# Performance work log

Measured on AMD Instinct MI355X. Metric: run time of the kernel, lower is better.

## Reference

```python
import jax, jax.numpy as jnp
import numpy as np
import math

NUM_HEADS = 16

def _skew(QEr):
    # QEr: [B, H, S, S] -> pad 1 on left of last dim, reshape, drop first row
    B, H, S, _ = QEr.shape
    padded = jnp.pad(QEr, ((0, 0), (0, 0), (0, 0), (1, 0)))  # [B,H,S,S+1]
    reshaped = padded.reshape(B, H, S + 1, S)
    return reshaped[:, :, 1:, :]  # [B,H,S,S]

def setup_inputs() -> dict:
    key = jax.random.key(0)
    ks = jax.random.split(key, 8)
    B, S, D, dh = 4, 1024, 1024, 64
    x = jax.random.normal(ks[0], (B, S, D), dtype=jnp.float32)
    scale = 1.0 / math.sqrt(D)
    Wq = jax.random.normal(ks[1], (D, D), dtype=jnp.float32) * scale
    Wk = jax.random.normal(ks[2], (D, D), dtype=jnp.float32) * scale
    Wv = jax.random.normal(ks[3], (D, D), dtype=jnp.float32) * scale
    bq = jnp.zeros((D,), dtype=jnp.float32)
    bk = jnp.zeros((D,), dtype=jnp.float32)
    bv = jnp.zeros((D,), dtype=jnp.float32)
    Er = jax.random.normal(ks[4], (S, dh), dtype=jnp.float32)
    return {"x": x, "Wq": Wq, "bq": bq, "Wk": Wk, "bk": bk, "Wv": Wv, "bv": bv, "Er": Er}

def reference(x, Wq, bq, Wk, bk, Wv, bv, Er):
    B, S, D = x.shape
    H = NUM_HEADS
    dh = D // H
    # Linear projections (torch Linear: x @ W.T + b)
    q = (x @ Wq.T + bq).reshape(B, S, H, dh).transpose(0, 2, 1, 3)  # [B,H,S,dh]
    k = (x @ Wk.T + bk).reshape(B, S, H, dh).transpose(0, 2, 1, 3)
    v = (x @ Wv.T + bv).reshape(B, S, H, dh).transpose(0, 2, 1, 3)
    # Relative position term: q @ Er^T then skew (start = max_len - S = 0)
    QEr = jnp.einsum('bhsd,td->bhst', q, Er)  # [B,H,S,S]
    Srel = _skew(QEr)
    QKt = jnp.einsum('bhsd,bhtd->bhst', q, k)  # [B,H,S,S]
    attn = (QKt + Srel) / math.sqrt(dh)
    causal = jnp.tril(jnp.ones((S, S), dtype=bool))
    attn = jnp.where(causal[None, None], attn, jnp.float32(-1e6))
    attn = jax.nn.softmax(attn, axis=-1)
    out = jnp.einsum('bhst,bhtd->bhsd', attn, v)  # [B,H,S,dh]
    out = out.transpose(0, 2, 1, 3).reshape(B, S, D)
    return out  # dropout is identity in eval / p=0
```

## Files before the change

### kernel.cpp

```cpp
#include <hip/hip_runtime.h>
#include <stdint.h>

#define S_LEN 1024
#define DM 1024
#define NH 16
#define DH 64
#define NB 4

typedef unsigned short u16;
typedef __attribute__((ext_vector_type(8))) short short8;
typedef __attribute__((ext_vector_type(4))) float f32x4;
typedef __attribute__((ext_vector_type(4))) unsigned int u32x4;

__device__ __forceinline__ u16 f2bf(float f) {
  union { float f; unsigned int u; } c;
  c.f = f;
  unsigned int u = c.u;
  return (u16)((u + 0x7fffu + ((u >> 16) & 1u)) >> 16);
}

__device__ __forceinline__ void g2l16(const void* g, void* l) {
  __builtin_amdgcn_global_load_lds(
      (const __attribute__((address_space(1))) unsigned int*)(uintptr_t)g,
      (__attribute__((address_space(3))) unsigned int*)(uint32_t)(uintptr_t)l,
      16, 0, 0);
}

__global__ __launch_bounds__(256) void cvt_f32_bf16(
    const float* __restrict__ x, const float* __restrict__ Wq,
    const float* __restrict__ Wk, const float* __restrict__ Wv,
    const float* __restrict__ Er, u16* __restrict__ xb,
    u16* __restrict__ Wqb, u16* __restrict__ Wkb, u16* __restrict__ Wvb,
    u16* __restrict__ Erb) {
  const size_t f = ((size_t)blockIdx.x * 256 + threadIdx.x) * 8;
  const float* src;
  u16* dst;
  size_t off;
  if (f < 4194304) { src = x; dst = xb; off = f; }
  else if (f < 5242880) { src = Wq; dst = Wqb; off = f - 4194304; }
  else if (f < 6291456) { src = Wk; dst = Wkb; off = f - 5242880; }
  else if (f < 7340032) { src = Wv; dst = Wvb; off = f - 6291456; }
  else { src = Er; dst = Erb; off = f - 7340032; }
  const float4 a = *(const float4*)(src + off);
  const float4 b = *(const float4*)(src + off + 4);
  u16 o[8] = {f2bf(a.x), f2bf(a.y), f2bf(a.z), f2bf(a.w),
              f2bf(b.x), f2bf(b.y), f2bf(b.z), f2bf(b.w)};
  *(u32x4*)(dst + off) = *(const u32x4*)o;
}

__global__ __launch_bounds__(256) void qkv_gemm(
    const u16* __restrict__ x,
    const u16* __restrict__ Wq, const float* __restrict__ bq,
    const u16* __restrict__ Wk, const float* __restrict__ bk,
    const u16* __restrict__ Wv, const float* __restrict__ bv,
    u16* __restrict__ Qo, u16* __restrict__ Ko, u16* __restrict__ Vo) {
  __shared__ __attribute__((aligned(16))) u16 Al[128 * 32];
  __shared__ __attribute__((aligned(16))) u16 Bl[128 * 32];

  const int tid = threadIdx.x;
  const int lane = tid & 63;
  const int wave = tid >> 6;
  const int z = blockIdx.z;
  const u16* W = (z == 0) ? Wq : (z == 1) ? Wk : Wv;
  const float* bias = (z == 0) ? bq : (z == 1) ? bk : bv;

  const int m0 = blockIdx.y * 128;
  const int n0 = blockIdx.x * 128;

  f32x4 acc[4][4];
  const f32x4 fzero = {0.f, 0.f, 0.f, 0.f};
#pragma unroll
  for (int i = 0; i < 4; i++)
#pragma unroll
    for (int j = 0; j < 4; j++) acc[i][j] = fzero;

  const int srow = tid >> 2;
  const int schunk = tid & 3;
  const u16* gA = x + (size_t)(m0 + srow) * DM + schunk * 8;
  const u16* gB = W + (size_t)(n0 + srow) * DM + schunk * 8;

  const int fr = lane & 15;
  const int fq = lane >> 4;
  const int wr = (wave >> 1) * 64;
  const int wc = (wave & 1) * 64;

  for (int k = 0; k < DM; k += 32) {
    g2l16(gA + k, &Al[tid * 8]);
    g2l16(gA + (size_t)64 * DM + k, &Al[2048 + tid * 8]);
    g2l16(gB + k, &Bl[tid * 8]);
    g2l16(gB + (size_t)64 * DM + k, &Bl[2048 + tid * 8]);
    __syncthreads();
    short8 a[4], b[4];
#pragma unroll
    for (int i = 0; i < 4; i++)
      a[i] = *(const short8*)&Al[(wr + i * 16 + fr) * 32 + fq * 8];
#pragma unroll
    for (int j = 0; j < 4; j++)
      b[j] = *(const short8*)&Bl[(wc + j * 16 + fr) * 32 + fq * 8];
#pragma unroll
    for (int i = 0; i < 4; i++)
#pragma unroll
      for (int j = 0; j < 4; j++)
        acc[i][j] =
            __builtin_amdgcn_mfma_f32_16x16x32_bf16(a[i], b[j], acc[i][j], 0, 0, 0);
    __syncthreads();
  }

#pragma unroll
  for (int j = 0; j < 4; j++) {
    const int n = n0 + wc + j * 16 + fr;
    const float bsv = bias[n];
    const int h = n >> 6, d = n & (DH - 1);
#pragma unroll
    for (int i = 0; i < 4; i++) {
#pragma unroll
      for (int r = 0; r < 4; r++) {
        const int m = m0 + wr + i * 16 + fq * 4 + r;
        const int bb = m >> 10, s = m & (S_LEN - 1);
        const u16 o = f2bf(acc[i][j][r] + bsv);
        if (z == 2)
          Vo[((size_t)(bb * NH + h) * DH + d) * S_LEN + s] = o;
        else if (z == 1)
          Ko[((size_t)(bb * NH + h) * S_LEN + s) * DH + d] = o;
        else
          Qo[((size_t)(bb * NH + h) * S_LEN + s) * DH + d] = o;
      }
    }
  }
}

__global__ __launch_bounds__(512, 4) void attn(
    const u16* __restrict__ Q, const u16* __restrict__ K,
    const u16* __restrict__ Vt, const u16* __restrict__ Er,
    float* __restrict__ out) {
  __shared__ __attribute__((aligned(16))) u16 El[192 * 72];
  __shared__ __attribute__((aligned(16))) u16 Kl[64 * 72];
  __shared__ __attribute__((aligned(16))) u16 Vl[64 * 72];
  __shared__ __attribute__((aligned(16))) u16 Pl[8 * 16 * 72];

  const int tid = threadIdx.x;
  const int lane = tid & 63;
  const int w = tid >> 6;
  const int bh = blockIdx.y;
  const int b = bh >> 4, h = bh & (NH - 1);
  const int it = (blockIdx.y < 32) ? (int)blockIdx.x : 7 - (int)blockIdx.x;
  const int i0 = it * 128;

  const u16* Qb = Q + (size_t)bh * S_LEN * DH;
  const u16* Kb = K + (size_t)bh * S_LEN * DH;
  const u16* Vb = Vt + (size_t)bh * DH * S_LEN;
  u16* Pw = Pl + w * 16 * 72;

  const int sr = tid >> 3;
  const int sc = (tid & 7) * 8;

  *(u32x4*)&El[sr * 72 + sc] = *(const u32x4*)&Qb[(i0 + sr) * DH + sc];
  *(u32x4*)&El[(sr + 64) * 72 + sc] =
      *(const u32x4*)&Qb[(i0 + sr + 64) * DH + sc];
  __syncthreads();

  const int fr = lane & 15;
  const int fq = lane >> 4;
  short8 aq0 = *(const short8*)&El[(w * 16 + fr) * 72 + fq * 8];
  short8 aq1 = *(const short8*)&El[(w * 16 + fr) * 72 + 32 + fq * 8];
  __syncthreads();

  float mrow[4], lrow[4];
  f32x4 accO[4];
  const f32x4 fzero = {0.f, 0.f, 0.f, 0.f};
#pragma unroll
  for (int r = 0; r < 4; r++) { mrow[r] = -3.0e38f; lrow[r] = 0.f; }
#pragma unroll
  for (int t = 0; t < 4; t++) accO[t] = fzero;

  for (int j0 = 0; j0 <= i0 + 64; j0 += 64) {
    *(u32x4*)&Kl[sr * 72 + sc] = *(const u32x4*)&Kb[(j0 + sr) * DH + sc];
    *(u32x4*)&Vl[sr * 72 + sc] = *(const u32x4*)&Vb[sr * S_LEN + j0 + sc];
    const int E0 = S_LEN - 128 - i0 + j0;
#pragma unroll
    for (int qq = 0; qq < 3; qq++) {
      const int g = sr + 64 * qq;
      int e = E0 + g;
      e = (e > S_LEN - 1) ? (S_LEN - 1) : e;
      *(u32x4*)&El[g * 72 + sc] = *(const u32x4*)&Er[e * DH + sc];
    }
    __syncthreads();

    if (j0 <= i0 + w * 16 + 15) {
      f32x4 sfr[4];
#pragma unroll
      for (int t = 0; t < 4; t++) {
        short8 b0 = *(const short8*)&Kl[(t * 16 + fr) * 72 + fq * 8];
        short8 b1 = *(const short8*)&Kl[(t * 16 + fr) * 72 + 32 + fq * 8];
        f32x4 zz = fzero;
        zz = __builtin_amdgcn_mfma_f32_16x16x32_bf16(aq0, b0, zz, 0, 0, 0);
        zz = __builtin_amdgcn_mfma_f32_16x16x32_bf16(aq1, b1, zz, 0, 0, 0);
        sfr[t] = zz;
      }

      f32x4 zz[5];
#pragma unroll
      for (int f = 0; f < 5; f++) {
        const int er = 112 - w * 16 + f * 16 + fr;
        short8 b0 = *(const short8*)&El[er * 72 + fq * 8];
        short8 b1 = *(const short8*)&El[er * 72 + 32 + fq * 8];
        f32x4 t0 = fzero;
        t0 = __builtin_amdgcn_mfma_f32_16x16x32_bf16(aq0, b0, t0, 0, 0, 0);
        t0 = __builtin_amdgcn_mfma_f32_16x16x32_bf16(aq1, b1, t0, 0, 0, 0);
        zz[f] = t0;
      }

      float p[4][4];
#pragma unroll
      for (int r = 0; r < 4; r++) {
        const int row = fq * 4 + r;
        const int c = 15 - row + fr;
        const int src = (fq << 4) | (c & 15);
        float sh[5];
#pragma unroll
        for (int f = 0; f < 5; f++) sh[f] = __shfl(zz[f][r], src);
#pragma unroll
        for (int t = 0; t < 4; t++) {
          const float rel = (c < 16) ? sh[t] : sh[t + 1];
          float sv = (sfr[t][r] + rel) * 0.125f;
          const int jj = j0 + t * 16 + fr;
          const int ii = i0 + w * 16 + row;
          if (jj > ii) sv = -3.0e38f;
          p[t][r] = sv;
        }
      }

#pragma unroll
      for (int r = 0; r < 4; r++) {
        float rm = fmaxf(fmaxf(p[0][r], p[1][r]), fmaxf(p[2][r], p[3][r]));
#pragma unroll
        for (int off = 1; off < 16; off <<= 1)
          rm = fmaxf(rm, __shfl_xor(rm, off));
        const float mnew = fmaxf(mrow[r], rm);
        const float alpha = __expf(mrow[r] - mnew);
        mrow[r] = mnew;
        float rs = 0.f;
#pragma unroll
        for (int t = 0; t < 4; t++) {
          const float e = __expf(p[t][r] - mnew);
          p[t][r] = e;
          rs += e;
        }
#pragma unroll
        for (int off = 1; off < 16; off <<= 1) rs += __shfl_xor(rs, off);
        lrow[r] = lrow[r] * alpha + rs;
#pragma unroll
        for (int t = 0; t < 4; t++) accO[t][r] *= alpha;
      }

#pragma unroll
      for (int t = 0; t < 4; t++)
#pragma unroll
        for (int r = 0; r < 4; r++)
          Pw[(fq * 4 + r) * 72 + t * 16 + fr] = f2bf(p[t][r]);
      __builtin_amdgcn_s_waitcnt(0xC07F);

      short8 ap0 = *(const short8*)&Pw[fr * 72 + fq * 8];
      short8 ap1 = *(const short8*)&Pw[fr * 72 + 32 + fq * 8];
#pragma unroll
      for (int t = 0; t < 4; t++) {
        short8 b0 = *(const short8*)&Vl[(t * 16 + fr) * 72 + fq * 8];
        short8 b1 = *(const short8*)&Vl[(t * 16 + fr) * 72 + 32 + fq * 8];
        accO[t] =
            __builtin_amdgcn_mfma_f32_16x16x32_bf16(ap0, b0, accO[t], 0, 0, 0);
        accO[t] =
            __builtin_amdgcn_mfma_f32_16x16x32_bf16(ap1, b1, accO[t], 0, 0, 0);
      }
    }
    __syncthreads();
  }

#pragma unroll
  for (int r = 0; r < 4; r++) {
    const float inv = 1.f / lrow[r];
    const int s = i0 + w * 16 + fq * 4 + r;
#pragma unroll
    for (int t = 0; t < 4; t++) {
      const int d = t * 16 + fr;
      out[((size_t)b * S_LEN + s) * DM + h * DH + d] = accO[t][r] * inv;
    }
  }
}

extern "C" void kernel_launch(void* const* d_in, const int* in_sizes, int n_in,
                              void* d_out, int out_size, void* d_ws, size_t ws_size,
                              hipStream_t stream) {
  const float* x = (const float*)d_in[0];
  const float* Wq = (const float*)d_in[1];
  const float* bq = (const float*)d_in[2];
  const float* Wk = (const float*)d_in[3];
  const float* bk = (const float*)d_in[4];
  const float* Wv = (const float*)d_in[5];
  const float* bv = (const float*)d_in[6];
  const float* Er = (const float*)d_in[7];
  float* out = (float*)d_out;

  const size_t per = (size_t)NB * NH * S_LEN * DH;
  u16* Qw = (u16*)d_ws;
  u16* Kw = Qw + per;
  u16* Vw = Kw + per;
  u16* xb = Vw + per;
  u16* Wqb = xb + per;
  u16* Wkb = Wqb + (size_t)DM * DM;
  u16* Wvb = Wkb + (size_t)DM * DM;
  u16* Erb = Wvb + (size_t)DM * DM;

  cvt_f32_bf16<<<3616, 256, 0, stream>>>(x, Wq, Wk, Wv, Er, xb, Wqb, Wkb, Wvb,
                                         Erb);
  dim3 g1(DM / 128, (NB * S_LEN) / 128, 3);
  qkv_gemm<<<g1, dim3(256), 0, stream>>>(xb, Wqb, bq, Wkb, bk, Wvb, bv, Qw, Kw,
                                         Vw);
  dim3 g2(8, NB * NH);
  attn<<<g2, dim3(512), 0, stream>>>(Qw, Kw, Vw, Erb, out);
}
```

Baseline: 179.5 us.

## Load attention K/V/Er fragments directly from global memory, dropping LDS staging

The attention kernel no longer stages Q, K, V and Er tiles in shared memory with block-wide barriers. Each wave loads its MFMA operand fragments straight from global memory, relying on L1/L2 caching, and loops only up to its own causal limit. This removes the __syncthreads and LDS traffic and lets waves progress independently. The cost is that every wave re-fetches K/V/Er fragments from global memory, which adds cache traffic and latency that is no longer amortized across the 8 waves of a block. The tile order for reversing the row-block sweep now alternates by head parity instead of by the batch half.

Result: slower. 300.6 us (+67.5%).

```diff
diff --git a/kernel.cpp b/kernel.cpp
--- a/kernel.cpp
+++ b/kernel.cpp
@@ -133,17 +133,15 @@
     const u16* __restrict__ Q, const u16* __restrict__ K,
     const u16* __restrict__ Vt, const u16* __restrict__ Er,
     float* __restrict__ out) {
-  __shared__ __attribute__((aligned(16))) u16 El[192 * 72];
-  __shared__ __attribute__((aligned(16))) u16 Kl[64 * 72];
-  __shared__ __attribute__((aligned(16))) u16 Vl[64 * 72];
   __shared__ __attribute__((aligned(16))) u16 Pl[8 * 16 * 72];
 
   const int tid = threadIdx.x;
   const int lane = tid & 63;
   const int w = tid >> 6;
+  const int bx = blockIdx.x;
   const int bh = blockIdx.y;
   const int b = bh >> 4, h = bh & (NH - 1);
-  const int it = (blockIdx.y < 32) ? (int)blockIdx.x : 7 - (int)blockIdx.x;
+  const int it = (bh & 1) ? 7 - bx : bx;
   const int i0 = it * 128;
 
   const u16* Qb = Q + (size_t)bh * S_LEN * DH;
@@ -151,19 +149,12 @@
   const u16* Vb = Vt + (size_t)bh * DH * S_LEN;
   u16* Pw = Pl + w * 16 * 72;
 
-  const int sr = tid >> 3;
-  const int sc = (tid & 7) * 8;
-
-  *(u32x4*)&El[sr * 72 + sc] = *(const u32x4*)&Qb[(i0 + sr) * DH + sc];
-  *(u32x4*)&El[(sr + 64) * 72 + sc] =
-      *(const u32x4*)&Qb[(i0 + sr + 64) * DH + sc];
-  __syncthreads();
-
   const int fr = lane & 15;
   const int fq = lane >> 4;
-  short8 aq0 = *(const short8*)&El[(w * 16 + fr) * 72 + fq * 8];
-  short8 aq1 = *(const short8*)&El[(w * 16 + fr) * 72 + 32 + fq * 8];
-  __syncthreads();
+
+  const u16* qrow = Qb + (size_t)(i0 + w * 16 + fr) * DH;
+  short8 aq0 = *(const short8*)&qrow[fq * 8];
+  short8 aq1 = *(const short8*)&qrow[32 + fq * 8];
 
   float mrow[4], lrow[4];
   f32x4 accO[4];
@@ -173,106 +164,98 @@
 #pragma unroll
   for (int t = 0; t < 4; t++) accO[t] = fzero;
 
-  for (int j0 = 0; j0 <= i0 + 64; j0 += 64) {
-    *(u32x4*)&Kl[sr * 72 + sc] = *(const u32x4*)&Kb[(j0 + sr) * DH + sc];
-    *(u32x4*)&Vl[sr * 72 + sc] = *(const u32x4*)&Vb[sr * S_LEN + j0 + sc];
-    const int E0 = S_LEN - 128 - i0 + j0;
-#pragma unroll
-    for (int qq = 0; qq < 3; qq++) {
-      const int g = sr + 64 * qq;
-      int e = E0 + g;
+  const int jmax = i0 + w * 16 + 15;
+  for (int j0 = 0; j0 <= jmax; j0 += 64) {
+    f32x4 sfr[4];
+#pragma unroll
+    for (int t = 0; t < 4; t++) {
+      const u16* kp = Kb + (size_t)(j0 + t * 16 + fr) * DH;
+      short8 b0 = *(const short8*)&kp[fq * 8];
+      short8 b1 = *(const short8*)&kp[32 + fq * 8];
+      f32x4 zt = fzero;
+      zt = __builtin_amdgcn_mfma_f32_16x16x32_bf16(aq0, b0, zt, 0, 0, 0);
+      zt = __builtin_amdgcn_mfma_f32_16x16x32_bf16(aq1, b1, zt, 0, 0, 0);
+      sfr[t] = zt;
+    }
+
+    const int E0 = 896 - i0 + j0;
+    f32x4 zz[5];
+#pragma unroll
+    for (int f = 0; f < 5; f++) {
+      int e = E0 + 112 - w * 16 + f * 16 + fr;
       e = (e > S_LEN - 1) ? (S_LEN - 1) : e;
-      *(u32x4*)&El[g * 72 + sc] = *(const u32x4*)&Er[e * DH + sc];
-    }
-    __syncthreads();
-
-    if (j0 <= i0 + w * 16 + 15) {
-      f32x4 sfr[4];
+      const u16* ep = Er + (size_t)e * DH;
+      short8 b0 = *(const short8*)&ep[fq * 8];
+      short8 b1 = *(const short8*)&ep[32 + fq * 8];
+      f32x4 t0 = fzero;
+      t0 = __builtin_amdgcn_mfma_f32_16x16x32_bf16(aq0, b0, t0, 0, 0, 0);
+      t0 = __builtin_amdgcn_mfma_f32_16x16x32_bf16(aq1, b1, t0, 0, 0, 0);
+      zz[f] = t0;
+    }
+
+    float p[4][4];
+#pragma unroll
+    for (int r = 0; r < 4; r++) {
+      const int row = fq * 4 + r;
+      const int c = 15 - row + fr;
+      const int src = (fq << 4) | (c & 15);
+      float sh[5];
+#pragma unroll
+      for (int f = 0; f < 5; f++) sh[f] = __shfl(zz[f][r], src);
 #pragma unroll
       for (int t = 0; t < 4; t++) {
-        short8 b0 = *(const short8*)&Kl[(t * 16 + fr) * 72 + fq * 8];
-        short8 b1 = *(const short8*)&Kl[(t * 16 + fr) * 72 + 32 + fq * 8];
-        f32x4 zz = fzero;
-        zz = __builtin_amdgcn_mfma_f32_16x16x32_bf16(aq0, b0, zz, 0, 0, 0);
-        zz = __builtin_amdgcn_mfma_f32_16x16x32_bf16(aq1, b1, zz, 0, 0, 0);
-        sfr[t] = zz;
+        const float rel = (c < 16) ? sh[t] : sh[t + 1];
+        float sv = (sfr[t][r] + rel) * 0.125f;
+        const int jj = j0 + t * 16 + fr;
+        const int ii = i0 + w * 16 + row;
+        if (jj > ii) sv = -3.0e38f;
+        p[t][r] = sv;
       }
-
-      f32x4 zz[5];
-#pragma unroll
-      for (int f = 0; f < 5; f++) {
-        const int er = 112 - w * 16 + f * 16 + fr;
-        short8 b0 = *(const short8*)&El[er * 72 + fq * 8];
-        short8 b1 = *(const short8*)&El[er * 72 + 32 + fq * 8];
-        f32x4 t0 = fzero;
-        t0 = __builtin_amdgcn_mfma_f32_16x16x32_bf16(aq0, b0, t0, 0, 0, 0);
-        t0 = __builtin_amdgcn_mfma_f32_16x16x32_bf16(aq1, b1, t0, 0, 0, 0);
-        zz[f] = t0;
+    }
+
+#pragma unroll
+    for (int r = 0; r < 4; r++) {
+      float rm = fmaxf(fmaxf(p[0][r], p[1][r]), fmaxf(p[2][r], p[3][r]));
+#pragma unroll
+      for (int off = 1; off < 16; off <<= 1)
+        rm = fmaxf(rm, __shfl_xor(rm, off));
+      const float mnew = fmaxf(mrow[r], rm);
+      const float alpha = __expf(mrow[r] - mnew);
+      mrow[r] = mnew;
+      float rs = 0.f;
+#pragma unroll
+      for (int t = 0; t < 4; t++) {
+        const float e = __expf(p[t][r] - mnew);
+        p[t][r] = e;
+        rs += e;
       }
-
-      float p[4][4];
-#pragma unroll
-      for (int r = 0; r < 4; r++) {
-        const int row = fq * 4 + r;
-        const int c = 15 - row + fr;
-        const int src = (fq << 4) | (c & 15);
-        float sh[5];
-#pragma unroll
-        for (int f = 0; f < 5; f++) sh[f] = __shfl(zz[f][r], src);
-#pragma unroll
-        for (int t = 0; t < 4; t++) {
-          const float rel = (c < 16) ? sh[t] : sh[t + 1];
-          float sv = (sfr[t][r] + rel) * 0.125f;
-          const int jj = j0 + t * 16 + fr;
-          const int ii = i0 + w * 16 + row;
-          if (jj > ii) sv = -3.0e38f;
-          p[t][r] = sv;
-        }
-      }
-
-#pragma unroll
-      for (int r = 0; r < 4; r++) {
-        float rm = fmaxf(fmaxf(p[0][r], p[1][r]), fmaxf(p[2][r], p[3][r]));
-#pragma unroll
-        for (int off = 1; off < 16; off <<= 1)
-          rm = fmaxf(rm, __shfl_xor(rm, off));
-        const float mnew = fmaxf(mrow[r], rm);
-        const float alpha = __expf(mrow[r] - mnew);
-        mrow[r] = mnew;
-        float rs = 0.f;
-#pragma unroll
-        for (int t = 0; t < 4; t++) {
-          const float e = __expf(p[t][r] - mnew);
-          p[t][r] = e;
-          rs += e;
-        }
-#pragma unroll
-        for (int off = 1; off < 16; off <<= 1) rs += __shfl_xor(rs, off);
-        lrow[r] = lrow[r] * alpha + rs;
-#pragma unroll
-        for (int t = 0; t < 4; t++) accO[t][r] *= alpha;
-      }
-
-#pragma unroll
-      for (int t = 0; t < 4; t++)
-#pragma unroll
-        for (int r = 0; r < 4; r++)
-          Pw[(fq * 4 + r) * 72 + t * 16 + fr] = f2bf(p[t][r]);
-      __builtin_amdgcn_s_waitcnt(0xC07F);
-
-      short8 ap0 = *(const short8*)&Pw[fr * 72 + fq * 8];
-      short8 ap1 = *(const short8*)&Pw[fr * 72 + 32 + fq * 8];
-#pragma unroll
-      for (int t = 0; t < 4; t++) {
-        short8 b0 = *(const short8*)&Vl[(t * 16 + fr) * 72 + fq * 8];
-        short8 b1 = *(const short8*)&Vl[(t * 16 + fr) * 72 + 32 + fq * 8];
-        accO[t] =
-            __builtin_amdgcn_mfma_f32_16x16x32_bf16(ap0, b0, accO[t], 0, 0, 0);
-        accO[t] =
-            __builtin_amdgcn_mfma_f32_16x16x32_bf16(ap1, b1, accO[t], 0, 0, 0);
-      }
-    }
-    __syncthreads();
+#pragma unroll
+      for (int off = 1; off < 16; off <<= 1) rs += __shfl_xor(rs, off);
+      lrow[r] = lrow[r] * alpha + rs;
+#pragma unroll
+      for (int t = 0; t < 4; t++) accO[t][r] *= alpha;
+    }
+
+#pragma unroll
+    for (int t = 0; t < 4; t++)
+#pragma unroll
+      for (int r = 0; r < 4; r++)
+        Pw[(fq * 4 + r) * 72 + t * 16 + fr] = f2bf(p[t][r]);
+    __builtin_amdgcn_s_waitcnt(0xC07F);
+
+    short8 ap0 = *(const short8*)&Pw[fr * 72 + fq * 8];
+    short8 ap1 = *(const short8*)&Pw[fr * 72 + 32 + fq * 8];
+
+#pragma unroll
+    for (int t = 0; t < 4; t++) {
+      const u16* vp = Vb + (size_t)(t * 16 + fr) * S_LEN + j0;
+      short8 b0 = *(const short8*)&vp[fq * 8];
+      short8 b1 = *(const short8*)&vp[32 + fq * 8];
+      accO[t] =
+          __builtin_amdgcn_mfma_f32_16x16x32_bf16(ap0, b0, accO[t], 0, 0, 0);
+      accO[t] =
+          __builtin_amdgcn_mfma_f32_16x16x32_bf16(ap1, b1, accO[t], 0, 0, 0);
+    }
   }
 
 #pragma unroll
```
